# Performance work log

Hardware: AMD Instinct MI355X
Metric: run time of the kernel (lower is better)

Reference implementation:

```python
import jax, jax.numpy as jnp
import numpy as np

EPS = 1e-6


def smooth(p):
    # smooth_distribution: clamp Bernoulli params away from {0,1}
    return jnp.clip(p, EPS, 1.0 - EPS)


def bern_logprob(p, x):
    # Bernoulli(p).log_prob(x) = x*log(p) + (1-x)*log(1-p)
    return x * jnp.log(p) + (1.0 - x) * jnp.log1p(-p)


def binary_row_reduce(A, b, k):
    # GF(2) Gaussian elimination on [A | b]; A:(k,n) binary float, b:(k,)
    M = jnp.concatenate([A, b[:, None]], axis=1)  # (k, n+1)
    rows = jnp.arange(k)
    for i in range(k):  # k is a small static int (25)
        col = M[:, i]
        cand = jnp.where((rows >= i) & (col > 0.5), rows, k)
        p = jnp.minimum(jnp.min(cand), k - 1)  # pivot row (fallback k-1 if none; prob ~0 for random A)
        ri, rp = M[i], M[p]
        M = M.at[i].set(rp)
        M = M.at[p].set(ri)
        elim = (M[:, i] > 0.5) & (rows != i)
        M = jnp.where(elim[:, None], jnp.mod(M + M[i], 2.0), M)
    return M[:, :-1], M[:, -1]


def compute_term1(logq, logp):
    # stable [sum_s q*log p]/[sum_s q], summed over batch; logq,logp: (S,B)
    m = jnp.max(logq, axis=0)                                  # (B,)
    w = jnp.exp(logq - m)                                      # (S,B)
    neg_num = m + jnp.log(jnp.sum(w * (-logp), axis=0))
    pos_den = m + jnp.log(jnp.sum(w, axis=0))
    return -jnp.sum(jnp.exp(neg_num - pos_den))


def setup_inputs() -> dict:
    key = jax.random.key(0)
    ks = jax.random.split(key, 5)
    nx, nz, B = 2048, 256, 512
    wr = float(np.sqrt(6.0 / (nx + nz)))
    xr = float(np.sqrt(6.0 / nx))
    zr = float(np.sqrt(6.0 / nz))
    U = jax.random.uniform(ks[0], (nz, nx), minval=-wr, maxval=wr)
    V = jax.random.uniform(ks[1], (nx, nz), minval=-wr, maxval=wr)
    x_bias = jax.random.uniform(ks[2], (nx,), minval=-xr, maxval=xr)
    z_bias = jax.random.uniform(ks[3], (nz,), minval=-zr, maxval=zr)
    xin = (jax.random.uniform(ks[4], (B, nx)) < 0.5).astype(jnp.float32)
    return {"xin": xin, "U": U, "V": V, "x_bias": x_bias, "z_bias": z_bias,
            "S": 10, "k": 25, "T": 30}


def reference(xin, U, V, x_bias, z_bias, S, k, T):
    dt = xin.dtype
    key = jax.random.key(42)
    kz, kx, kA, kb = jax.random.split(key, 4)

    # q(z|x) and samples  -------------------------------------------------
    q = smooth(jax.nn.sigmoid(xin @ U.T + z_bias))                     # (B, nz)
    samples_z = (jax.random.uniform(kz, (S,) + q.shape) < q).astype(dt)  # (S,B,nz)
    ps = smooth(jax.nn.sigmoid(jnp.einsum('sbz,xz->sbx', samples_z, V) + x_bias))  # (S,B,nx)
    xouts = (jax.random.uniform(kx, ps.shape) < ps).astype(dt)

    # projected ELBO over T random GF(2) hash constraints ------------------
    nz = U.shape[0]
    A_all = (jax.random.uniform(kA, (T, k, nz)) < 0.5).astype(dt)
    b_all = (jax.random.uniform(kb, (T, k)) < 0.5).astype(dt)
    pz = smooth(jax.nn.sigmoid(z_bias))                                # (nz,)

    def elbo_t(carry, Ab):
        A, b = Ab
        C, bp = binary_row_reduce(A, b, k)                             # (k,nz),(k,)
        proj = jnp.mod(jnp.einsum('sbz,kz->sbk', samples_z[:, :, k:], C[:, k:]) + bp, 2.0)
        sz = samples_z.at[:, :, :k].set(proj)                          # (S,B,nz)
        logq_zi = bern_logprob(q, sz).sum(axis=2)                      # (S,B)
        logp_z = bern_logprob(pz, sz).sum(axis=2)                      # (S,B)
        ps_t = smooth(jax.nn.sigmoid(jnp.einsum('sbz,xz->sbx', sz, V) + x_bias))
        logp_x = bern_logprob(ps_t, xin).sum(axis=2)                   # (S,B)
        logp = logp_z + logp_x
        term2 = compute_term1(logq_zi, logq_zi)
        term1 = compute_term1(logq_zi, logp)
        return carry, term1 - term2

    _, pelbos = jax.lax.scan(elbo_t, 0.0, (A_all, b_all))
    loss = -jnp.mean(pelbos)
    return q, samples_z, ps, xouts, loss
```

## Files before the change

kernel.cpp:

```cpp
#include <hip/hip_runtime.h>
#include <cstdint>

#define NX 2048
#define NZ 256
#define NB 512
#define NS 10
#define NK 25
#define NT 30
#define SBTOT (NS * NB)

#define LOG2E 1.4426950408889634f
#define LN2 0.6931471805599453f

#define OFF_Q 0
#define OFF_SAMP (NB * NZ)
#define OFF_PS (OFF_SAMP + SBTOT * NZ)
#define OFF_XO (OFF_PS + SBTOT * NX)
#define OFF_LOSS (OFF_XO + SBTOT * NX)

typedef unsigned long long ull;
typedef __bf16 bf16x8 __attribute__((ext_vector_type(8)));
typedef float f32x4 __attribute__((ext_vector_type(4)));

__host__ __device__ inline void tf2x32(uint32_t k0, uint32_t k1, uint32_t x0, uint32_t x1,
                                       uint32_t& o0, uint32_t& o1) {
  uint32_t k2 = k0 ^ k1 ^ 0x1BD11BDAu;
  x0 += k0; x1 += k1;
#define TF_R(r) { x0 += x1; x1 = (x1 << (r)) | (x1 >> (32 - (r))); x1 ^= x0; }
  TF_R(13) TF_R(15) TF_R(26) TF_R(6)
  x0 += k1; x1 += k2 + 1u;
  TF_R(17) TF_R(29) TF_R(16) TF_R(24)
  x0 += k2; x1 += k0 + 2u;
  TF_R(13) TF_R(15) TF_R(26) TF_R(6)
  x0 += k0; x1 += k1 + 3u;
  TF_R(17) TF_R(29) TF_R(16) TF_R(24)
  x0 += k1; x1 += k2 + 4u;
  TF_R(13) TF_R(15) TF_R(26) TF_R(6)
  x0 += k2; x1 += k0 + 5u;
#undef TF_R
  o0 = x0; o1 = x1;
}

__device__ inline uint32_t tf_select(uint32_t k0, uint32_t k1, uint32_t i, uint32_t h) {
  bool lo = i < h;
  uint32_t x0 = lo ? i : i - h;
  uint32_t x1 = lo ? i + h : i;
  uint32_t o0, o1;
  tf2x32(k0, k1, x0, x1, o0, o1);
  return lo ? o0 : o1;
}

__device__ inline float tf_uniform(uint32_t k0, uint32_t k1, uint32_t i, uint32_t h) {
  uint32_t r = tf_select(k0, k1, i, h);
  return __uint_as_float(0x3f800000u | (r >> 9)) - 1.0f;
}

__device__ inline float sigclip(float a) {
  float p = 1.0f / (1.0f + __expf(-a));
  return fminf(fmaxf(p, 1e-6f), 1.0f - 1e-6f);
}

__device__ inline ushort f2bf(float f) {
  uint32_t u = __float_as_uint(f);
  return (ushort)((u + 0x7FFFu + ((u >> 16) & 1u)) >> 16);
}

__device__ inline float blockReduceSum256(float v, volatile float* s4) {
#pragma unroll
  for (int o = 32; o > 0; o >>= 1) v += __shfl_down(v, o);
  __syncthreads();
  if ((threadIdx.x & 63) == 0) s4[threadIdx.x >> 6] = v;
  __syncthreads();
  return s4[0] + s4[1] + s4[2] + s4[3];
}

__global__ __launch_bounds__(256) void kP0_prep(const float* __restrict__ V,
                                                const float* __restrict__ U,
                                                const float* __restrict__ xin,
                                                const float* __restrict__ z_bias,
                                                ushort* __restrict__ Vbf,
                                                ushort* __restrict__ Vkpad2,
                                                ushort* __restrict__ Uhi,
                                                ushort* __restrict__ Ulo,
                                                ushort* __restrict__ xinbf,
                                                float* __restrict__ baseq,
                                                float* __restrict__ d_lpz,
                                                float* __restrict__ basepz) {
  __shared__ float red[4];
  int e = blockIdx.x * 256 + threadIdx.x;
  {
    int x = e >> 8, k = e & 255;
    float v = V[e];
    Vbf[e] = f2bf(v);
    if (k < 32) Vkpad2[x * 32 + k] = (k < NK) ? f2bf(v * LOG2E) : (ushort)0;
  }
  {
    float u = U[e];
    ushort hi = f2bf(u);
    Uhi[e] = hi;
    float hv = __uint_as_float((uint32_t)hi << 16);
    Ulo[e] = f2bf(u - hv);
  }
  {
    xinbf[e] = (xin[e] > 0.5f) ? (ushort)0x3F80 : (ushort)0;
    int e2 = e + NX * NZ;
    xinbf[e2] = (xin[e2] > 0.5f) ? (ushort)0x3F80 : (ushort)0;
  }
  if (e < NB) baseq[e] = 0.0f;
  if (blockIdx.x == 0) {
    int z = threadIdx.x;
    float pz = sigclip(z_bias[z]);
    float lp = __logf(pz), l1 = __logf(1.0f - pz);
    d_lpz[z] = lp - l1;
    float s = blockReduceSum256(l1, red);
    if (z == 0) *basepz = s;
  }
}

__global__ __launch_bounds__(256) void kW_signdot(const float* __restrict__ xin,
                                                  const ushort* __restrict__ Vkpad2,
                                                  float* __restrict__ W) {
  __shared__ float wred[4][NK];
  int b = blockIdx.x;
  int tid = threadIdx.x;
  float acc[NK];
#pragma unroll
  for (int j = 0; j < NK; ++j) acc[j] = 0.0f;
#pragma unroll
  for (int i = 0; i < 8; ++i) {
    int x = i * 256 + tid;
    float s = 1.0f - 2.0f * xin[(size_t)b * NX + x];
    const uint4* vp = (const uint4*)(Vkpad2 + (size_t)x * 32);
    uint4 q0 = vp[0], q1 = vp[1], q2 = vp[2], q3 = vp[3];
    uint32_t w[16] = {q0.x, q0.y, q0.z, q0.w, q1.x, q1.y, q1.z, q1.w,
                      q2.x, q2.y, q2.z, q2.w, q3.x, q3.y, q3.z, q3.w};
#pragma unroll
    for (int j = 0; j < NK; ++j) {
      uint32_t wd = w[j >> 1];
      float v = __uint_as_float((j & 1) ? (wd & 0xFFFF0000u) : (wd << 16));
      acc[j] = fmaf(s, v, acc[j]);
    }
  }
#pragma unroll
  for (int j = 0; j < NK; ++j) {
#pragma unroll
    for (int o = 1; o < 64; o <<= 1) acc[j] += __shfl_xor(acc[j], o);
  }
  if ((tid & 63) == 0) {
#pragma unroll
    for (int j = 0; j < NK; ++j) wred[tid >> 6][j] = acc[j];
  }
  __syncthreads();
  if (tid < NK) W[b * 32 + tid] = wred[0][tid] + wred[1][tid] + wred[2][tid] + wred[3][tid];
}

__global__ __launch_bounds__(256) void k1a_mfma(const ushort* __restrict__ xinbf,
                                                const ushort* __restrict__ Uhi,
                                                const ushort* __restrict__ Ulo,
                                                const float* __restrict__ z_bias,
                                                float* __restrict__ outq,
                                                float* __restrict__ d_lq,
                                                float* __restrict__ baseq) {
  __shared__ float red[4][16][17];
  int tid = threadIdx.x;
  int wave = tid >> 6, lane = tid & 63, grp = lane >> 4, col = lane & 15;
  int b0 = (blockIdx.x >> 4) * 16;
  int z0 = (blockIdx.x & 15) * 16;
  f32x4 acc = {0.f, 0.f, 0.f, 0.f};
  const ushort* arow = xinbf + (size_t)(b0 + col) * NX + wave * 512 + grp * 8;
  const ushort* bhr = Uhi + (size_t)(z0 + col) * NX + wave * 512 + grp * 8;
  const ushort* blr = Ulo + (size_t)(z0 + col) * NX + wave * 512 + grp * 8;
#pragma unroll 4
  for (int s = 0; s < 16; ++s) {
    bf16x8 a = *(const bf16x8*)(arow + s * 32);
    bf16x8 bh = *(const bf16x8*)(bhr + s * 32);
    bf16x8 bl = *(const bf16x8*)(blr + s * 32);
    acc = __builtin_amdgcn_mfma_f32_16x16x32_bf16(a, bh, acc, 0, 0, 0);
    acc = __builtin_amdgcn_mfma_f32_16x16x32_bf16(a, bl, acc, 0, 0, 0);
  }
#pragma unroll
  for (int r = 0; r < 4; ++r) red[wave][grp * 4 + r][col] = acc[r];
  __syncthreads();
  int bi = tid >> 4, zi = tid & 15;
  float aa = red[0][bi][zi] + red[1][bi][zi] + red[2][bi][zi] + red[3][bi][zi] + z_bias[z0 + zi];
  int b = b0 + bi, z = z0 + zi;
  float q = sigclip(aa);
  outq[b * NZ + z] = q;
  float lq = __logf(q), l1 = __logf(1.0f - q);
  d_lq[b * NZ + z] = lq - l1;
  float s1 = l1;
#pragma unroll
  for (int o = 1; o < 16; o <<= 1) s1 += __shfl_xor(s1, o);
  if (zi == 0) atomicAdd(&baseq[b], s1);
}

__global__ __launch_bounds__(256) void k2_samples(const float* __restrict__ q,
                                                  const float* __restrict__ d_lq,
                                                  const float* __restrict__ d_lpz,
                                                  float* __restrict__ samp_out,
                                                  ushort* __restrict__ samp16,
                                                  ull* __restrict__ Spack,
                                                  float* __restrict__ qtail,
                                                  float* __restrict__ ptail,
                                                  uint32_t kz0, uint32_t kz1) {
  __shared__ float red[4];
  int sb = blockIdx.x;
  int z = threadIdx.x;
  int b = sb & (NB - 1);
  uint32_t i = (uint32_t)sb * NZ + z;
  const uint32_t h = (uint32_t)SBTOT * NZ / 2;
  float u = tf_uniform(kz0, kz1, i, h);
  float qv = q[b * NZ + z];
  int smp = (u < qv) ? 1 : 0;
  samp_out[i] = (float)smp;
  samp16[i] = smp ? (ushort)0x3F80 : (ushort)0;
  ull m = __ballot(smp);
  if ((z & 63) == 0) Spack[sb * 4 + (z >> 6)] = m;
  float dq = (z >= NK && smp) ? d_lq[b * NZ + z] : 0.0f;
  float dp = (z >= NK && smp) ? d_lpz[z] : 0.0f;
  float sq = blockReduceSum256(dq, red);
  float sp = blockReduceSum256(dp, red);
  if (z == 0) { qtail[sb] = sq; ptail[sb] = sp; }
}

__global__ __launch_bounds__(256) void k3m_gemm(const ushort* __restrict__ samp16,
                                                const ushort* __restrict__ Vbf,
                                                const float* __restrict__ x_bias,
                                                ushort* __restrict__ base2,
                                                float* __restrict__ ps_out,
                                                float* __restrict__ xo_out,
                                                uint32_t kx0, uint32_t kx1) {
  __shared__ __align__(16) char smem[2 * 2112 * 4];
  ushort* As = (ushort*)smem;
  ushort* Bs = (ushort*)(smem + 8192);
  float* Tt = (float*)smem;

  int tid = threadIdx.x;
  int wave = tid >> 6, lane = tid & 63, grp = lane >> 4, col = lane & 15;
  int x0 = blockIdx.x * 128;
  int sb0 = blockIdx.y * 32;
  f32x4 acc[2][4];
#pragma unroll
  for (int mi = 0; mi < 2; ++mi)
#pragma unroll
    for (int ni = 0; ni < 4; ++ni) acc[mi][ni] = (f32x4){0.f, 0.f, 0.f, 0.f};

  for (int k0 = 0; k0 < NZ; k0 += 32) {
    {
      int rowb = tid >> 2, kcb = (tid & 3) << 3;
      int sbrow = (rowb < 32) ? (sb0 + rowb) : (sb0 + 2528 + rowb);
      *(uint4*)&Bs[rowb * 32 + kcb] = *(const uint4*)&samp16[(size_t)sbrow * NZ + k0 + kcb];
#pragma unroll
      for (int c = tid; c < 512; c += 256) {
        int rowa = c >> 2, kca = (c & 3) << 3;
        *(uint4*)&As[rowa * 32 + kca] = *(const uint4*)&Vbf[(size_t)(x0 + rowa) * NZ + k0 + kca];
      }
    }
    __syncthreads();
    bf16x8 af[2], bfv[4];
#pragma unroll
    for (int mi = 0; mi < 2; ++mi)
      af[mi] = *(const bf16x8*)&As[(wave * 32 + mi * 16 + col) * 32 + grp * 8];
#pragma unroll
    for (int ni = 0; ni < 4; ++ni)
      bfv[ni] = *(const bf16x8*)&Bs[(ni * 16 + col) * 32 + grp * 8];
#pragma unroll
    for (int mi = 0; mi < 2; ++mi)
#pragma unroll
      for (int ni = 0; ni < 4; ++ni)
        acc[mi][ni] = __builtin_amdgcn_mfma_f32_16x16x32_bf16(af[mi], bfv[ni], acc[mi][ni], 0, 0, 0);
    __syncthreads();
  }

  const uint32_t HH = (uint32_t)(SBTOT / 2) * (uint32_t)NX;
#pragma unroll
  for (int pi = 0; pi < 2; ++pi) {
    __syncthreads();
#pragma unroll
    for (int mi = 0; mi < 2; ++mi) {
      int cbase = wave * 32 + mi * 16 + grp * 4;
      *(float4*)&Tt[col * 132 + cbase] = *(float4*)&acc[mi][pi];
      *(float4*)&Tt[2112 + col * 132 + cbase] = *(float4*)&acc[mi][pi + 2];
    }
    __syncthreads();
#pragma unroll
    for (int pass = 0; pass < 2; ++pass) {
      int r = pass * 8 + (tid >> 5);
      int c = (tid & 31) * 4;
      float4 t0 = *(float4*)&Tt[r * 132 + c];
      float4 t1 = *(float4*)&Tt[2112 + r * 132 + c];
      float4 xb4 = *(const float4*)(x_bias + x0 + c);
      int sb_a = sb0 + pi * 16 + r;
      size_t off_a = (size_t)sb_a * NX + x0 + c;
      size_t off_b = off_a + (size_t)HH;
      float a0 = t0.x + xb4.x, a1 = t0.y + xb4.y, a2 = t0.z + xb4.z, a3 = t0.w + xb4.w;
      float b0 = t1.x + xb4.x, b1 = t1.y + xb4.y, b2 = t1.z + xb4.z, b3 = t1.w + xb4.w;
      uint2 bpa, bpb;
      bpa.x = (uint32_t)f2bf(a0 * LOG2E) | ((uint32_t)f2bf(a1 * LOG2E) << 16);
      bpa.y = (uint32_t)f2bf(a2 * LOG2E) | ((uint32_t)f2bf(a3 * LOG2E) << 16);
      bpb.x = (uint32_t)f2bf(b0 * LOG2E) | ((uint32_t)f2bf(b1 * LOG2E) << 16);
      bpb.y = (uint32_t)f2bf(b2 * LOG2E) | ((uint32_t)f2bf(b3 * LOG2E) << 16);
      *(uint2*)(base2 + off_a) = bpa;
      *(uint2*)(base2 + off_b) = bpb;
      float4 pva = make_float4(sigclip(a0), sigclip(a1), sigclip(a2), sigclip(a3));
      float4 pvb = make_float4(sigclip(b0), sigclip(b1), sigclip(b2), sigclip(b3));
      *(float4*)(ps_out + off_a) = pva;
      *(float4*)(ps_out + off_b) = pvb;
      uint32_t fi = (uint32_t)off_a;
      uint32_t r0, r1;
      float4 xva, xvb;
      tf2x32(kx0, kx1, fi + 0u, fi + 0u + HH, r0, r1);
      xva.x = ((__uint_as_float(0x3f800000u | (r0 >> 9)) - 1.0f) < pva.x) ? 1.0f : 0.0f;
      xvb.x = ((__uint_as_float(0x3f800000u | (r1 >> 9)) - 1.0f) < pvb.x) ? 1.0f : 0.0f;
      tf2x32(kx0, kx1, fi + 1u, fi + 1u + HH, r0, r1);
      xva.y = ((__uint_as_float(0x3f800000u | (r0 >> 9)) - 1.0f) < pva.y) ? 1.0f : 0.0f;
      xvb.y = ((__uint_as_float(0x3f800000u | (r1 >> 9)) - 1.0f) < pvb.y) ? 1.0f : 0.0f;
      tf2x32(kx0, kx1, fi + 2u, fi + 2u + HH, r0, r1);
      xva.z = ((__uint_as_float(0x3f800000u | (r0 >> 9)) - 1.0f) < pva.z) ? 1.0f : 0.0f;
      xvb.z = ((__uint_as_float(0x3f800000u | (r1 >> 9)) - 1.0f) < pvb.z) ? 1.0f : 0.0f;
      tf2x32(kx0, kx1, fi + 3u, fi + 3u + HH, r0, r1);
      xva.w = ((__uint_as_float(0x3f800000u | (r0 >> 9)) - 1.0f) < pva.w) ? 1.0f : 0.0f;
      xvb.w = ((__uint_as_float(0x3f800000u | (r1 >> 9)) - 1.0f) < pvb.w) ? 1.0f : 0.0f;
      *(float4*)(xo_out + off_a) = xva;
      *(float4*)(xo_out + off_b) = xvb;
    }
  }
}

__global__ __launch_bounds__(256) void k4_rowreduce(ull* __restrict__ Ct,
                                                    uint32_t* __restrict__ bpmask,
                                                    uint32_t kA0, uint32_t kA1,
                                                    uint32_t kb0, uint32_t kb1) {
  __shared__ uint32_t Aw[NK][8];
  __shared__ uint32_t bbsh[NK];
  int t = blockIdx.x;
  int tid = threadIdx.x;
  if (tid < NK * 8) {
    int r = tid >> 3, c = tid & 7;
    const uint32_t hA = (uint32_t)NT * NK * NZ / 2;
    uint32_t base_i = (uint32_t)(t * NK + r) * NZ + c * 32;
    uint32_t w = 0;
    for (int zz = 0; zz < 32; ++zz) {
      uint32_t rr = tf_select(kA0, kA1, base_i + zz, hA);
      w |= ((rr >> 31) ^ 1u) << zz;
    }
    Aw[r][c] = w;
  }
  if (tid < NK) {
    const uint32_t hb = (uint32_t)NT * NK / 2;
    uint32_t rb = tf_select(kb0, kb1, (uint32_t)(t * NK + tid), hb);
    bbsh[tid] = (rb >> 31) ^ 1u;
  }
  __syncthreads();
  if (tid >= 64) return;
  int lane = tid;
  ull w0 = 0, w1 = 0, w2 = 0, w3 = 0;
  uint32_t bbit = 0;
  if (lane < NK) {
    w0 = (ull)Aw[lane][0] | ((ull)Aw[lane][1] << 32);
    w1 = (ull)Aw[lane][2] | ((ull)Aw[lane][3] << 32);
    w2 = (ull)Aw[lane][4] | ((ull)Aw[lane][5] << 32);
    w3 = (ull)Aw[lane][6] | ((ull)Aw[lane][7] << 32);
    bbit = bbsh[lane];
  }
  for (int i = 0; i < NK; ++i) {
    int mybit = (int)((w0 >> i) & 1ull);
    ull mask = __ballot(lane < NK && mybit);
    ull cand = mask & (~0ull << i);
    int p = cand ? __builtin_ctzll(cand) : (NK - 1);
    int srcl = (lane == i) ? p : ((lane == p) ? i : lane);
    w0 = __shfl(w0, srcl); w1 = __shfl(w1, srcl); w2 = __shfl(w2, srcl); w3 = __shfl(w3, srcl);
    bbit = __shfl(bbit, srcl);
    ull p0 = __shfl(w0, i), p1 = __shfl(w1, i), p2 = __shfl(w2, i), p3 = __shfl(w3, i);
    uint32_t pvb = __shfl(bbit, i);
    int nb2 = (int)((w0 >> i) & 1ull);
    if (lane < NK && lane != i && nb2) {
      w0 ^= p0; w1 ^= p1; w2 ^= p2; w3 ^= p3; bbit ^= pvb;
    }
  }
  if (lane < NK) {
    w0 &= ~((1ull << NK) - 1ull);
    ull* dstp = Ct + (size_t)(t * NK + lane) * 4;
    dstp[0] = w0; dstp[1] = w1; dstp[2] = w2; dstp[3] = w3;
  }
  ull bm = __ballot(lane < NK && bbit);
  if (lane == 0) bpmask[t] = (uint32_t)bm & 0x1FFFFFFu;
}

__global__ __launch_bounds__(256) void k5_proj(const ull* __restrict__ Spack,
                                               const ull* __restrict__ Ct,
                                               const uint32_t* __restrict__ bpmask,
                                               const float* __restrict__ W,
                                               uint32_t* __restrict__ projb,
                                               float* __restrict__ Syd) {
  int e = blockIdx.x * 256 + threadIdx.x;
  int sb = e >> 5, t = e & 31;
  ull s0 = Spack[sb * 4 + 0], s1 = Spack[sb * 4 + 1];
  ull s2 = Spack[sb * 4 + 2], s3 = Spack[sb * 4 + 3];
  uint32_t s25 = (uint32_t)(s0 & 0x1FFFFFFull);
  const float* Wb = W + (size_t)(sb & (NB - 1)) * 32;
  uint32_t out;
  float syd = 0.0f;
  if (t < NT) {
    uint32_t bp = bpmask[t];
    uint32_t pb = 0;
#pragma unroll
    for (int j = 0; j < NK; ++j) {
      const ull* C = Ct + (size_t)(t * NK + j) * 4;
      int par = __popcll(s0 & C[0]) + __popcll(s1 & C[1]) + __popcll(s2 & C[2]) + __popcll(s3 & C[3]);
      uint32_t bit = ((uint32_t)(par ^ (int)(bp >> j))) & 1u;
      pb |= bit << j;
      int d = (int)bit - (int)((s25 >> j) & 1u);
      syd = fmaf((float)d, Wb[j], syd);
    }
    out = pb;
  } else {
    out = s25;
  }
  projb[e] = out;
  Syd[e] = syd;
}

__global__ __launch_bounds__(256) void k6_mfma(const ushort* __restrict__ base2,
                                               const ushort* __restrict__ Vkpad2,
                                               const float* __restrict__ xin,
                                               const uint32_t* __restrict__ projb,
                                               const ull* __restrict__ Spack,
                                               const float* __restrict__ Syd,
                                               float* __restrict__ logpx) {
  __shared__ float bvsm[NX];
  __shared__ float lsum[4][32];
  __shared__ float red[4];
  int sb = blockIdx.x;
  int b = sb & (NB - 1);
  int tid = threadIdx.x;
  int wave = tid >> 6, lane = tid & 63;
  int grp = lane >> 4, col = lane & 15;
  const uint4* b16p = (const uint4*)(base2 + (size_t)sb * NX);
  const float4* x4p = (const float4*)(xin + (size_t)b * NX);
  float sbacc = 0.0f;
  {
    uint4 bu = b16p[tid];
    float4 xv0 = x4p[tid * 2], xv1 = x4p[tid * 2 + 1];
    uint32_t wds[4] = {bu.x, bu.y, bu.z, bu.w};
    float bv[8];
#pragma unroll
    for (int j = 0; j < 8; ++j) {
      uint32_t wd = wds[j >> 1];
      bv[j] = __uint_as_float((j & 1) ? (wd & 0xFFFF0000u) : (wd << 16));
    }
    float sg[8] = {1.0f - 2.0f * xv0.x, 1.0f - 2.0f * xv0.y, 1.0f - 2.0f * xv0.z,
                   1.0f - 2.0f * xv0.w, 1.0f - 2.0f * xv1.x, 1.0f - 2.0f * xv1.y,
                   1.0f - 2.0f * xv1.z, 1.0f - 2.0f * xv1.w};
#pragma unroll
    for (int j = 0; j < 8; ++j) {
      bvsm[tid * 8 + j] = bv[j];
      sbacc = fmaf(sg[j], bv[j], sbacc);
    }
  }
  float Sb = blockReduceSum256(sbacc, red);
  uint32_t s25 = (uint32_t)(Spack[sb * 4] & 0x1FFFFFFull);
  uint32_t pb0 = projb[sb * 32 + col];
  uint32_t pb1 = projb[sb * 32 + 16 + col];
  bf16x8 a0, a1;
  union { ushort u; __bf16 hh; } cvt;
#pragma unroll
  for (int j = 0; j < 8; ++j) {
    int k = grp * 8 + j;
    int sbit = (int)((s25 >> k) & 1u);
    int d0 = (int)((pb0 >> k) & 1u) - sbit;
    int d1 = (int)((pb1 >> k) & 1u) - sbit;
    cvt.u = (ushort)(d0 == 0 ? 0 : (d0 > 0 ? 0x3F80 : 0xBF80)); a0[j] = cvt.hh;
    cvt.u = (ushort)(d1 == 0 ? 0 : (d1 > 0 ? 0x3F80 : 0xBF80)); a1[j] = cvt.hh;
  }
  float acca[8], pp[8];
#pragma unroll
  for (int r = 0; r < 8; ++r) { acca[r] = 0.0f; pp[r] = 1.0f; }
  const ushort* vkbase = Vkpad2 + (size_t)(wave * 512 + col) * 32 + grp * 8;
#pragma unroll 4
  for (int i = 0; i < 32; ++i) {
    int x = (wave * 32 + i) * 16 + col;
    bf16x8 bfr = *(const bf16x8*)(vkbase + (size_t)i * 16 * 32);
    f32x4 c0 = {0.f, 0.f, 0.f, 0.f}, c1 = {0.f, 0.f, 0.f, 0.f};
    c0 = __builtin_amdgcn_mfma_f32_16x16x32_bf16(a0, bfr, c0, 0, 0, 0);
    c1 = __builtin_amdgcn_mfma_f32_16x16x32_bf16(a1, bfr, c1, 0, 0, 0);
    float bs = bvsm[x];
#pragma unroll
    for (int r = 0; r < 4; ++r) {
      float y0 = bs + c0[r];
      acca[r] += fabsf(y0);
      pp[r] = fmaf(pp[r], __builtin_amdgcn_exp2f(-fabsf(y0)), pp[r]);
      float y1 = bs + c1[r];
      acca[4 + r] += fabsf(y1);
      pp[4 + r] = fmaf(pp[4 + r], __builtin_amdgcn_exp2f(-fabsf(y1)), pp[4 + r]);
    }
  }
#pragma unroll
  for (int r = 0; r < 8; ++r) {
    float m = 0.5f * acca[r] + __log2f(pp[r]);
#pragma unroll
    for (int off = 1; off < 16; off <<= 1) m += __shfl_xor(m, off);
    if (col == 0) {
      int t = (r < 4) ? (grp * 4 + r) : (16 + grp * 4 + (r - 4));
      lsum[wave][t] = m;
    }
  }
  __syncthreads();
  if (tid < NT) {
    float tot = lsum[0][tid] + lsum[1][tid] + lsum[2][tid] + lsum[3][tid];
    tot += 0.5f * (Sb + Syd[sb * 32 + tid]);
    logpx[(size_t)tid * SBTOT + sb] = -LN2 * tot;
  }
}

__global__ __launch_bounds__(512) void k7_reduce(const float* __restrict__ logpx,
                                                 const uint32_t* __restrict__ projb,
                                                 const float* __restrict__ qtail,
                                                 const float* __restrict__ ptail,
                                                 const float* __restrict__ baseq,
                                                 const float* __restrict__ d_lq,
                                                 const float* __restrict__ d_lpz,
                                                 const float* __restrict__ basepz,
                                                 double* __restrict__ pelbo) {
  __shared__ double red8[8];
  int t = blockIdx.x;
  int b = threadIdx.x;
  float dlq[NK];
#pragma unroll
  for (int j = 0; j < NK; ++j) dlq[j] = d_lq[b * NZ + j];
  float bq = baseq[b];
  float bpz = *basepz;
  float lq[NS], lp[NS];
#pragma unroll
  for (int s = 0; s < NS; ++s) {
    int sb = s * NB + b;
    uint32_t m = projb[sb * 32 + t];
    float sq = 0.0f, spv = 0.0f;
#pragma unroll
    for (int j = 0; j < NK; ++j) {
      float on = (float)((m >> j) & 1u);
      sq += on * dlq[j];
      spv += on * d_lpz[j];
    }
    lq[s] = bq + qtail[sb] + sq;
    lp[s] = logpx[t * SBTOT + sb] + bpz + ptail[sb] + spv;
  }
  float mx = lq[0];
#pragma unroll
  for (int s = 1; s < NS; ++s) mx = fmaxf(mx, lq[s]);
  float den = 0.0f, num = 0.0f;
#pragma unroll
  for (int s = 0; s < NS; ++s) {
    float w = __expf(lq[s] - mx);
    den += w;
    num += w * (lq[s] - lp[s]);
  }
  double v = (double)(num / den);
#pragma unroll
  for (int o = 32; o > 0; o >>= 1) v += __shfl_down(v, o);
  __syncthreads();
  if ((b & 63) == 0) red8[b >> 6] = v;
  __syncthreads();
  if (b == 0) {
    double s = 0.0;
    for (int i = 0; i < 8; ++i) s += red8[i];
    pelbo[t] = s;
  }
}

__global__ __launch_bounds__(64) void k8_loss(const double* __restrict__ pelbo,
                                              float* __restrict__ out_loss) {
  int t = threadIdx.x;
  double v = (t < NT) ? pelbo[t] : 0.0;
#pragma unroll
  for (int o = 32; o > 0; o >>= 1) v += __shfl_down(v, o);
  if (t == 0) *out_loss = (float)(v / (double)NT);
}

extern "C" void kernel_launch(void* const* d_in, const int* in_sizes, int n_in,
                              void* d_out, int out_size, void* d_ws, size_t ws_size,
                              hipStream_t stream) {
  const float* xin = (const float*)d_in[0];
  const float* U = (const float*)d_in[1];
  const float* V = (const float*)d_in[2];
  const float* x_bias = (const float*)d_in[3];
  const float* z_bias = (const float*)d_in[4];
  float* out = (float*)d_out;

  char* p = (char*)d_ws;
  ushort* base2 = (ushort*)p;             p += (size_t)SBTOT * NX * 2;
  float* d_lq = (float*)p;                p += (size_t)NB * NZ * 4;
  float* baseq = (float*)p;               p += (size_t)NB * 4;
  float* d_lpz = (float*)p;               p += (size_t)NZ * 4;
  float* basepz = (float*)p;              p += 16;
  ull* Spack = (ull*)p;                   p += (size_t)SBTOT * 4 * 8;
  float* qtail = (float*)p;               p += (size_t)SBTOT * 4;
  float* ptail = (float*)p;               p += (size_t)SBTOT * 4;
  ull* Ct = (ull*)p;                      p += (size_t)NT * NK * 4 * 8;
  uint32_t* bpm = (uint32_t*)p;           p += 128;
  uint32_t* projb = (uint32_t*)p;         p += (size_t)SBTOT * 32 * 4;
  float* Syd = (float*)p;                 p += (size_t)SBTOT * 32 * 4;
  float* logpx = (float*)p;               p += (size_t)NT * SBTOT * 4;
  double* pelbo = (double*)p;             p += (size_t)NT * 8;
  ushort* Vkpad2 = (ushort*)p;            p += (size_t)NX * 32 * 2;
  ushort* Vbf = (ushort*)p;               p += (size_t)NX * NZ * 2;
  ushort* samp16 = (ushort*)p;            p += (size_t)SBTOT * NZ * 2;
  float* W = (float*)p;                   p += (size_t)NB * 32 * 4;
  ushort* Uhi = (ushort*)p;               p += (size_t)NZ * NX * 2;
  ushort* Ulo = (ushort*)p;               p += (size_t)NZ * NX * 2;
  ushort* xinbf = (ushort*)p;             p += (size_t)NB * NX * 2;
  (void)ws_size; (void)in_sizes; (void)n_in; (void)out_size;

  uint32_t o0[4], o1[4];
  for (int j = 0; j < 4; ++j) tf2x32(0u, 42u, (uint32_t)j, (uint32_t)(4 + j), o0[j], o1[j]);
  uint32_t kz0 = o0[0], kz1 = o0[1];
  uint32_t kx0 = o0[2], kx1 = o0[3];
  uint32_t kA0 = o1[0], kA1 = o1[1];
  uint32_t kb0 = o1[2], kb1 = o1[3];

  kP0_prep<<<NX * NZ / 256, 256, 0, stream>>>(V, U, xin, z_bias, Vbf, Vkpad2,
                                              Uhi, Ulo, xinbf, baseq, d_lpz, basepz);
  k4_rowreduce<<<NT, 256, 0, stream>>>(Ct, bpm, kA0, kA1, kb0, kb1);
  k1a_mfma<<<512, 256, 0, stream>>>(xinbf, Uhi, Ulo, z_bias, out + OFF_Q, d_lq, baseq);
  kW_signdot<<<NB, 256, 0, stream>>>(xin, Vkpad2, W);
  k2_samples<<<SBTOT, 256, 0, stream>>>(out + OFF_Q, d_lq, d_lpz, out + OFF_SAMP,
                                        samp16, Spack, qtail, ptail, kz0, kz1);
  dim3 g3(NX / 128, SBTOT / 64);
  k3m_gemm<<<g3, 256, 0, stream>>>(samp16, Vbf, x_bias, base2,
                                   out + OFF_PS, out + OFF_XO, kx0, kx1);
  k5_proj<<<SBTOT * 32 / 256, 256, 0, stream>>>(Spack, Ct, bpm, W, projb, Syd);
  k6_mfma<<<SBTOT, 256, 0, stream>>>(base2, Vkpad2, xin, projb, Spack, Syd, logpx);
  k7_reduce<<<NT, 512, 0, stream>>>(logpx, projb, qtail, ptail, baseq, d_lq,
                                    d_lpz, basepz, pelbo);
  k8_loss<<<1, 64, 0, stream>>>(pelbo, out + OFF_LOSS);
}
```

Baseline: 265.0 us.

## Fuse projection into sampling kernel, prefetch MFMA operands, split final reduce

The GF(2) projection (k5_proj) now runs inside k2_samples, reading the packed sample bits from shared memory, which removes one launch and a global round trip through Spack. In k6_mfma the next Vkpad2 fragment is loaded one iteration ahead and the unroll depth goes up, to hide load latency behind the MFMAs. k7_reduce is split across 8 chunks of 64 batch elements per t, so 240 small blocks replace 30 large ones, and k8_loss adds up the partial sums. The risks are extra serial work for 32 threads at the end of k2 and higher register pressure in k6.

```diff
diff --git a/kernel.cpp b/kernel.cpp
--- a/kernel.cpp
+++ b/kernel.cpp
@@ -197,13 +197,19 @@
 __global__ __launch_bounds__(256) void k2_samples(const float* __restrict__ q,
                                                   const float* __restrict__ d_lq,
                                                   const float* __restrict__ d_lpz,
+                                                  const ull* __restrict__ Ct,
+                                                  const uint32_t* __restrict__ bpmask,
+                                                  const float* __restrict__ W,
                                                   float* __restrict__ samp_out,
                                                   ushort* __restrict__ samp16,
                                                   ull* __restrict__ Spack,
                                                   float* __restrict__ qtail,
                                                   float* __restrict__ ptail,
+                                                  uint32_t* __restrict__ projb,
+                                                  float* __restrict__ Syd,
                                                   uint32_t kz0, uint32_t kz1) {
   __shared__ float red[4];
+  __shared__ ull sp_sh[4];
   int sb = blockIdx.x;
   int z = threadIdx.x;
   int b = sb & (NB - 1);
@@ -215,12 +221,38 @@
   samp_out[i] = (float)smp;
   samp16[i] = smp ? (ushort)0x3F80 : (ushort)0;
   ull m = __ballot(smp);
-  if ((z & 63) == 0) Spack[sb * 4 + (z >> 6)] = m;
+  if ((z & 63) == 0) { Spack[sb * 4 + (z >> 6)] = m; sp_sh[z >> 6] = m; }
   float dq = (z >= NK && smp) ? d_lq[b * NZ + z] : 0.0f;
   float dp = (z >= NK && smp) ? d_lpz[z] : 0.0f;
   float sq = blockReduceSum256(dq, red);
   float sp = blockReduceSum256(dp, red);
   if (z == 0) { qtail[sb] = sq; ptail[sb] = sp; }
+  if (z < 32) {
+    int t = z;
+    ull s0 = sp_sh[0], s1 = sp_sh[1], s2 = sp_sh[2], s3 = sp_sh[3];
+    uint32_t s25 = (uint32_t)(s0 & 0x1FFFFFFull);
+    const float* Wb = W + (size_t)b * 32;
+    uint32_t out;
+    float syd = 0.0f;
+    if (t < NT) {
+      uint32_t bp = bpmask[t];
+      uint32_t pb = 0;
+#pragma unroll
+      for (int j = 0; j < NK; ++j) {
+        const ull* C = Ct + (size_t)(t * NK + j) * 4;
+        int par = __popcll(s0 & C[0]) + __popcll(s1 & C[1]) + __popcll(s2 & C[2]) + __popcll(s3 & C[3]);
+        uint32_t bit = ((uint32_t)(par ^ (int)(bp >> j))) & 1u;
+        pb |= bit << j;
+        int d = (int)bit - (int)((s25 >> j) & 1u);
+        syd = fmaf((float)d, Wb[j], syd);
+      }
+      out = pb;
+    } else {
+      out = s25;
+    }
+    projb[sb * 32 + t] = out;
+    Syd[sb * 32 + t] = syd;
+  }
 }
 
 __global__ __launch_bounds__(256) void k3m_gemm(const ushort* __restrict__ samp16,
@@ -387,40 +419,6 @@
   if (lane == 0) bpmask[t] = (uint32_t)bm & 0x1FFFFFFu;
 }
 
-__global__ __launch_bounds__(256) void k5_proj(const ull* __restrict__ Spack,
-                                               const ull* __restrict__ Ct,
-                                               const uint32_t* __restrict__ bpmask,
-                                               const float* __restrict__ W,
-                                               uint32_t* __restrict__ projb,
-                                               float* __restrict__ Syd) {
-  int e = blockIdx.x * 256 + threadIdx.x;
-  int sb = e >> 5, t = e & 31;
-  ull s0 = Spack[sb * 4 + 0], s1 = Spack[sb * 4 + 1];
-  ull s2 = Spack[sb * 4 + 2], s3 = Spack[sb * 4 + 3];
-  uint32_t s25 = (uint32_t)(s0 & 0x1FFFFFFull);
-  const float* Wb = W + (size_t)(sb & (NB - 1)) * 32;
-  uint32_t out;
-  float syd = 0.0f;
-  if (t < NT) {
-    uint32_t bp = bpmask[t];
-    uint32_t pb = 0;
-#pragma unroll
-    for (int j = 0; j < NK; ++j) {
-      const ull* C = Ct + (size_t)(t * NK + j) * 4;
-      int par = __popcll(s0 & C[0]) + __popcll(s1 & C[1]) + __popcll(s2 & C[2]) + __popcll(s3 & C[3]);
-      uint32_t bit = ((uint32_t)(par ^ (int)(bp >> j))) & 1u;
-      pb |= bit << j;
-      int d = (int)bit - (int)((s25 >> j) & 1u);
-      syd = fmaf((float)d, Wb[j], syd);
-    }
-    out = pb;
-  } else {
-    out = s25;
-  }
-  projb[e] = out;
-  Syd[e] = syd;
-}
-
 __global__ __launch_bounds__(256) void k6_mfma(const ushort* __restrict__ base2,
                                                const ushort* __restrict__ Vkpad2,
                                                const float* __restrict__ xin,
@@ -476,15 +474,17 @@
   float acca[8], pp[8];
 #pragma unroll
   for (int r = 0; r < 8; ++r) { acca[r] = 0.0f; pp[r] = 1.0f; }
-  const ushort* vkbase = Vkpad2 + (size_t)(wave * 512 + col) * 32 + grp * 8;
-#pragma unroll 4
+  const ushort* vkp = Vkpad2 + (size_t)(wave * 512 + col) * 32 + grp * 8;
+  const float* bvp = bvsm + wave * 512 + col;
+  bf16x8 bcur = *(const bf16x8*)(vkp);
+#pragma unroll 8
   for (int i = 0; i < 32; ++i) {
-    int x = (wave * 32 + i) * 16 + col;
-    bf16x8 bfr = *(const bf16x8*)(vkbase + (size_t)i * 16 * 32);
+    bf16x8 bnxt = bcur;
+    if (i < 31) bnxt = *(const bf16x8*)(vkp + (size_t)(i + 1) * 512);
     f32x4 c0 = {0.f, 0.f, 0.f, 0.f}, c1 = {0.f, 0.f, 0.f, 0.f};
-    c0 = __builtin_amdgcn_mfma_f32_16x16x32_bf16(a0, bfr, c0, 0, 0, 0);
-    c1 = __builtin_amdgcn_mfma_f32_16x16x32_bf16(a1, bfr, c1, 0, 0, 0);
-    float bs = bvsm[x];
+    c0 = __builtin_amdgcn_mfma_f32_16x16x32_bf16(a0, bcur, c0, 0, 0, 0);
+    c1 = __builtin_amdgcn_mfma_f32_16x16x32_bf16(a1, bcur, c1, 0, 0, 0);
+    float bs = bvp[i * 16];
 #pragma unroll
     for (int r = 0; r < 4; ++r) {
       float y0 = bs + c0[r];
@@ -494,6 +494,7 @@
       acca[4 + r] += fabsf(y1);
       pp[4 + r] = fmaf(pp[4 + r], __builtin_amdgcn_exp2f(-fabsf(y1)), pp[4 + r]);
     }
+    bcur = bnxt;
   }
 #pragma unroll
   for (int r = 0; r < 8; ++r) {
@@ -513,18 +514,19 @@
   }
 }
 
-__global__ __launch_bounds__(512) void k7_reduce(const float* __restrict__ logpx,
-                                                 const uint32_t* __restrict__ projb,
-                                                 const float* __restrict__ qtail,
-                                                 const float* __restrict__ ptail,
-                                                 const float* __restrict__ baseq,
-                                                 const float* __restrict__ d_lq,
-                                                 const float* __restrict__ d_lpz,
-                                                 const float* __restrict__ basepz,
-                                                 double* __restrict__ pelbo) {
-  __shared__ double red8[8];
+__global__ __launch_bounds__(64) void k7_reduce(const float* __restrict__ logpx,
+                                                const uint32_t* __restrict__ projb,
+                                                const float* __restrict__ qtail,
+                                                const float* __restrict__ ptail,
+                                                const float* __restrict__ baseq,
+                                                const float* __restrict__ d_lq,
+                                                const float* __restrict__ d_lpz,
+                                                const float* __restrict__ basepz,
+                                                double* __restrict__ pelbo_part) {
   int t = blockIdx.x;
-  int b = threadIdx.x;
+  int chunk = blockIdx.y;
+  int lane = threadIdx.x;
+  int b = chunk * 64 + lane;
   float dlq[NK];
 #pragma unroll
   for (int j = 0; j < NK; ++j) dlq[j] = d_lq[b * NZ + j];
@@ -558,20 +560,17 @@
   double v = (double)(num / den);
 #pragma unroll
   for (int o = 32; o > 0; o >>= 1) v += __shfl_down(v, o);
-  __syncthreads();
-  if ((b & 63) == 0) red8[b >> 6] = v;
-  __syncthreads();
-  if (b == 0) {
-    double s = 0.0;
-    for (int i = 0; i < 8; ++i) s += red8[i];
-    pelbo[t] = s;
-  }
-}
-
-__global__ __launch_bounds__(64) void k8_loss(const double* __restrict__ pelbo,
+  if (lane == 0) pelbo_part[t * 8 + chunk] = v;
+}
+
+__global__ __launch_bounds__(64) void k8_loss(const double* __restrict__ pelbo_part,
                                               float* __restrict__ out_loss) {
   int t = threadIdx.x;
-  double v = (t < NT) ? pelbo[t] : 0.0;
+  double v = 0.0;
+  if (t < NT) {
+#pragma unroll
+    for (int c = 0; c < 8; ++c) v += pelbo_part[t * 8 + c];
+  }
 #pragma unroll
   for (int o = 32; o > 0; o >>= 1) v += __shfl_down(v, o);
   if (t == 0) *out_loss = (float)(v / (double)NT);
@@ -601,7 +600,7 @@
   uint32_t* projb = (uint32_t*)p;         p += (size_t)SBTOT * 32 * 4;
   float* Syd = (float*)p;                 p += (size_t)SBTOT * 32 * 4;
   float* logpx = (float*)p;               p += (size_t)NT * SBTOT * 4;
-  double* pelbo = (double*)p;             p += (size_t)NT * 8;
+  double* pelbo = (double*)p;             p += (size_t)NT * 8 * 8;
   ushort* Vkpad2 = (ushort*)p;            p += (size_t)NX * 32 * 2;
   ushort* Vbf = (ushort*)p;               p += (size_t)NX * NZ * 2;
   ushort* samp16 = (ushort*)p;            p += (size_t)SBTOT * NZ * 2;
@@ -623,14 +622,15 @@
   k4_rowreduce<<<NT, 256, 0, stream>>>(Ct, bpm, kA0, kA1, kb0, kb1);
   k1a_mfma<<<512, 256, 0, stream>>>(xinbf, Uhi, Ulo, z_bias, out + OFF_Q, d_lq, baseq);
   kW_signdot<<<NB, 256, 0, stream>>>(xin, Vkpad2, W);
-  k2_samples<<<SBTOT, 256, 0, stream>>>(out + OFF_Q, d_lq, d_lpz, out + OFF_SAMP,
-                                        samp16, Spack, qtail, ptail, kz0, kz1);
+  k2_samples<<<SBTOT, 256, 0, stream>>>(out + OFF_Q, d_lq, d_lpz, Ct, bpm, W,
+                                        out + OFF_SAMP, samp16, Spack, qtail, ptail,
+                                        projb, Syd, kz0, kz1);
   dim3 g3(NX / 128, SBTOT / 64);
   k3m_gemm<<<g3, 256, 0, stream>>>(samp16, Vbf, x_bias, base2,
                                    out + OFF_PS, out + OFF_XO, kx0, kx1);
-  k5_proj<<<SBTOT * 32 / 256, 256, 0, stream>>>(Spack, Ct, bpm, W, projb, Syd);
   k6_mfma<<<SBTOT, 256, 0, stream>>>(base2, Vkpad2, xin, projb, Spack, Syd, logpx);
-  k7_reduce<<<NT, 512, 0, stream>>>(logpx, projb, qtail, ptail, baseq, d_lq,
-                                    d_lpz, basepz, pelbo);
+  dim3 g7(NT, 8);
+  k7_reduce<<<g7, 64, 0, stream>>>(logpx, projb, qtail, ptail, baseq, d_lq,
+                                   d_lpz, basepz, pelbo);
   k8_loss<<<1, 64, 0, stream>>>(pelbo, out + OFF_LOSS);
 }
```

Measured after the change: 270.0 us. Within noise of the previous version (+1.9%).
